# Performance work log

Hardware: AMD Instinct MI355X
Metric: run time of the kernel (lower is better)

Reference implementation:

```python
import jax, jax.numpy as jnp
import numpy as np

H = 16      # num_attention_heads
D = 64      # attention_head_size
HID = H * D # hidden_size = 1024
N = 1024    # seq_len == max_len
K = 1024    # position_buckets == att_span (K >= N so un-clamped indices stay in range)
EPS = 1e-7  # layer_norm_eps


def setup_inputs() -> dict:
    key = jax.random.key(0)
    ks = jax.random.split(key, 12)

    def w(k, shape):
        return jax.random.normal(k, shape, dtype=jnp.float32) * 0.02

    return {
        "hidden_states": jax.random.normal(ks[0], (1, N, HID), dtype=jnp.float32),
        "rel_embeddings": jax.random.normal(ks[1], (2 * K, HID), dtype=jnp.float32),
        "Wq": w(ks[2], (HID, HID)), "bq": jnp.zeros((HID,), jnp.float32),
        "Wk": w(ks[3], (HID, HID)), "bk": jnp.zeros((HID,), jnp.float32),
        "Wv": w(ks[4], (HID, HID)), "bv": jnp.zeros((HID,), jnp.float32),
        "Wpk": w(ks[5], (HID, HID)), "bpk": jnp.zeros((HID,), jnp.float32),
        "Wpq": w(ks[6], (HID, HID)), "bpq": jnp.zeros((HID,), jnp.float32),
        "Wo": w(ks[7], (HID, HID)), "bo": jnp.zeros((HID,), jnp.float32),
        "ln_g": jnp.ones((HID,), jnp.float32),
        "ln_b": jnp.zeros((HID,), jnp.float32),
    }


def _heads(x):
    # (L, HID) -> (H, L, D)   (batch size is 1, matching the baked-in id offsets)
    L = x.shape[0]
    return x.reshape(L, H, D).transpose(1, 0, 2)


def reference(hidden_states, rel_embeddings, Wq, bq, Wk, bk, Wv, bv,
              Wpk, bpk, Wpq, bpq, Wo, bo, ln_g, ln_b):
    hs = hidden_states[0]                       # (N, HID)
    q = _heads(hs @ Wq.T + bq)                  # (H, N, D)
    k = _heads(hs @ Wk.T + bk)                  # (H, N, D)
    v = _heads(hs @ Wv.T + bv)                  # (H, N, D)

    scale = jnp.sqrt(jnp.asarray(D * 3, jnp.float32))  # scale_factor = 1 + c2p + p2c = 3
    scores = jnp.einsum('hid,hjd->hij', q, k) / scale  # (H, N, N)

    pos_k = _heads(rel_embeddings @ Wpk.T + bpk)       # (H, 2K, D)
    pos_q = _heads(rel_embeddings @ Wpq.T + bpq)       # (H, 2K, D)

    rows = jnp.arange(N)[:, None]                      # (N, 1)
    # ids[i, j] = (i - j) + K  (no clamp in the original; valid since K >= N)
    idx = K + jnp.arange(N)[:, None] - jnp.arange(N)[None, :]  # (N, N)

    # c2p: gather c2p_att[h, i, K + i - j]
    c2p_att = jnp.einsum('hid,hkd->hik', q, pos_k)     # (H, N, 2K)
    c2p = c2p_att[:, rows, idx]                        # (H, N, N)

    # p2c: gather p2c_att[h, i, K + j - i], then transpose last two dims
    p2c_att = jnp.einsum('hid,hkd->hik', k, pos_q)     # (H, N, 2K)
    p2c = jnp.swapaxes(p2c_att[:, rows, idx.T], -1, -2)  # (H, N, N)

    scores = scores + (c2p + p2c) / scale
    attn = jax.nn.softmax(scores, axis=-1)             # (H, N, N)

    ctx = jnp.einsum('hij,hjd->hid', attn, v)          # (H, N, D)
    ctx = ctx.transpose(1, 0, 2).reshape(1, N, HID)    # (1, N, HID)

    # DebertaV2SelfOutput: dense + residual LayerNorm
    out = ctx @ Wo.T + bo
    x = out + hidden_states
    mu = jnp.mean(x, axis=-1, keepdims=True)
    var = jnp.mean(jnp.square(x - mu), axis=-1, keepdims=True)
    return ((x - mu) / jnp.sqrt(var + EPS)) * ln_g + ln_b
```

## Files before the change

kernel.cpp:

```cpp
#include <hip/hip_runtime.h>
#include <stdint.h>

#define HID 1024
#define NSEQ 1024
#define KREL 1024
#define NHEAD 16
#define DHEAD 64

typedef __attribute__((ext_vector_type(8))) short bhalf8;
typedef __attribute__((ext_vector_type(4))) float floatx4;

typedef const __attribute__((address_space(1))) uint8_t* gas_t;
typedef __attribute__((address_space(3))) uint8_t* las_t;
__device__ inline void gload16(const void* g, void* l) {
  __builtin_amdgcn_global_load_lds((gas_t)g, (las_t)l, 16, 0, 0);
}

__device__ inline uint16_t f2bf(float f) {
  union { float f; uint32_t u; } c; c.f = f;
  uint32_t u = c.u;
  return (uint16_t)((u + 0x7fffu + ((u >> 16) & 1u)) >> 16);
}
__device__ inline uint32_t pkbf(float a, float b) {
  union { float f; uint32_t u; } x, y; x.f = a; y.f = b;
#if __has_builtin(__builtin_amdgcn_perm)
  return __builtin_amdgcn_perm(x.u + 0x8000u, y.u + 0x8000u, 0x03020706u);
#else
  return ((x.u + 0x8000u) >> 16) | ((y.u + 0x8000u) & 0xffff0000u);
#endif
}

struct Cast8 {
  const float* src[8];
  uint16_t* dst[8];
  int n[8];
};
__global__ __launch_bounds__(256) void cast8_kernel(Cast8 c) {
  int seg = blockIdx.y;
  int n = c.n[seg];
  const float* s = c.src[seg];
  uint16_t* d = c.dst[seg];
  for (int idx = (blockIdx.x * 256 + threadIdx.x) * 4; idx < n; idx += 1024 * 256 * 4) {
    float4 v = *(const float4*)(s + idx);
    ushort4 o;
    o.x = f2bf(v.x); o.y = f2bf(v.y); o.z = f2bf(v.z); o.w = f2bf(v.w);
    *(ushort4*)(d + idx) = o;
  }
}

struct ProjArgs {
  const uint16_t* A[5];
  const uint16_t* W[5];
  const float* bias[5];
  uint16_t* C[5];
  int trans[5];
};
__global__ __launch_bounds__(256) void proj_gemm(ProjArgs pa) {
  __shared__ uint16_t a_s[2][128 * 32];
  __shared__ uint16_t b_s[2][128 * 32];
  int bidx = blockIdx.x;
  int xcd = bidx & 7, idx = bidx >> 3;
  int g = xcd * 7 + (idx >> 3);
  int nt = idx & 7;
  int z, mt;
  if (g < 24) { z = g >> 3; mt = g & 7; }
  else { int g2 = g - 24; z = 3 + (g2 >> 4); mt = g2 & 15; }
  const uint16_t* A = pa.A[z];
  const uint16_t* W = pa.W[z];
  int i0 = mt * 128, n0 = nt * 128;

  int t = threadIdx.x;
  int lane = t & 63, w = t >> 6;
  int fm = lane & 15, kq = lane >> 4;
  int wm = (w >> 1) * 64, wn = (w & 1) * 64;

  int lr = t >> 2, lc = (t & 3) * 8;
  const uint16_t* Agl = A + (size_t)(i0 + lr) * HID + lc;
  const uint16_t* Wgl = W + (size_t)(n0 + lr) * HID + lc;
  int lofs = t * 8;

#define PSTAGE(BUF, K0)                                                    \
  do {                                                                     \
    gload16(Agl + (K0), &a_s[BUF][lofs]);                                  \
    gload16(Agl + (K0) + 64 * HID, &a_s[BUF][lofs + 2048]);                \
    gload16(Wgl + (K0), &b_s[BUF][lofs]);                                  \
    gload16(Wgl + (K0) + 64 * HID, &b_s[BUF][lofs + 2048]);                \
  } while (0)

  floatx4 acc[4][4] = {};

  PSTAGE(0, 0);
  __syncthreads();

  for (int kt = 0; kt < 32; ++kt) {
    int cur = kt & 1;
    if (kt < 31) PSTAGE(cur ^ 1, (kt + 1) * 32);
    const uint16_t* as = &a_s[cur][0];
    const uint16_t* bs = &b_s[cur][0];
    bhalf8 af[4], bf[4];
#pragma unroll
    for (int m2 = 0; m2 < 4; ++m2)
      af[m2] = *(bhalf8*)(as + (wm + m2 * 16 + fm) * 32 + kq * 8);
#pragma unroll
    for (int n2 = 0; n2 < 4; ++n2)
      bf[n2] = *(bhalf8*)(bs + (wn + n2 * 16 + fm) * 32 + kq * 8);
#pragma unroll
    for (int m2 = 0; m2 < 4; ++m2)
#pragma unroll
      for (int n2 = 0; n2 < 4; ++n2)
        acc[m2][n2] = __builtin_amdgcn_mfma_f32_16x16x32_bf16(af[m2], bf[n2], acc[m2][n2], 0, 0, 0);
    __syncthreads();
  }
#undef PSTAGE

  const float* bias = pa.bias[z];
  uint16_t* C = pa.C[z];
  int tr = pa.trans[z];
#pragma unroll
  for (int m2 = 0; m2 < 4; ++m2) {
    int rowb = i0 + wm + m2 * 16 + kq * 4;
#pragma unroll
    for (int n2 = 0; n2 < 4; ++n2) {
      int col = n0 + wn + n2 * 16 + fm;
      float bv = bias[col];
      floatx4 v = acc[m2][n2];
      if (tr) {
        uint2 p = { pkbf(v[0] + bv, v[1] + bv), pkbf(v[2] + bv, v[3] + bv) };
        *(uint2*)(C + (size_t)col * NSEQ + rowb) = p;
      } else {
#pragma unroll
        for (int r = 0; r < 4; ++r)
          C[(size_t)(rowb + r) * HID + col] = f2bf(v[r] + bv);
      }
    }
  }
}

__global__ __launch_bounds__(256) void out_gemm(const uint16_t* __restrict__ Abf,
                                                const uint16_t* __restrict__ W,
                                                const float* __restrict__ bias,
                                                float* __restrict__ C) {
  __shared__ uint16_t a_s[2][64 * 32];
  __shared__ uint16_t b_s[2][64 * 32];
  int bidx = blockIdx.x;
  int i0 = (bidx >> 4) * 64, n0 = (bidx & 15) * 64;
  int t = threadIdx.x;
  int lane = t & 63, w = t >> 6;
  int fm = lane & 15, kq = lane >> 4;
  int wm = (w >> 1) * 32, wn = (w & 1) * 32;
  int lr = t >> 2, lc = (t & 3) * 8;
  const uint16_t* Agl = Abf + (size_t)(i0 + lr) * HID + lc;
  const uint16_t* Wgl = W + (size_t)(n0 + lr) * HID + lc;
  int lofs = t * 8;

#define OSTAGE(BUF, K0)                                                    \
  do {                                                                     \
    gload16(Agl + (K0), &a_s[BUF][lofs]);                                  \
    gload16(Wgl + (K0), &b_s[BUF][lofs]);                                  \
  } while (0)

  floatx4 acc00 = {0,0,0,0}, acc01 = {0,0,0,0}, acc10 = {0,0,0,0}, acc11 = {0,0,0,0};
  OSTAGE(0, 0);
  __syncthreads();
  for (int kt = 0; kt < 32; ++kt) {
    int cur = kt & 1;
    if (kt < 31) OSTAGE(cur ^ 1, (kt + 1) * 32);
    const uint16_t* as = &a_s[cur][0];
    const uint16_t* bs = &b_s[cur][0];
    bhalf8 a0 = *(bhalf8*)(as + (wm + fm) * 32 + kq * 8);
    bhalf8 a1 = *(bhalf8*)(as + (wm + 16 + fm) * 32 + kq * 8);
    bhalf8 b0 = *(bhalf8*)(bs + (wn + fm) * 32 + kq * 8);
    bhalf8 b1 = *(bhalf8*)(bs + (wn + 16 + fm) * 32 + kq * 8);
    acc00 = __builtin_amdgcn_mfma_f32_16x16x32_bf16(a0, b0, acc00, 0, 0, 0);
    acc01 = __builtin_amdgcn_mfma_f32_16x16x32_bf16(a0, b1, acc01, 0, 0, 0);
    acc10 = __builtin_amdgcn_mfma_f32_16x16x32_bf16(a1, b0, acc10, 0, 0, 0);
    acc11 = __builtin_amdgcn_mfma_f32_16x16x32_bf16(a1, b1, acc11, 0, 0, 0);
    __syncthreads();
  }
#undef OSTAGE
  int rb0 = kq * 4;
#define EPO(ACC, SM, SN)                                                   \
  {                                                                        \
    int rowb = i0 + wm + (SM)*16 + rb0;                                    \
    int col = n0 + wn + (SN)*16 + fm;                                      \
    float bv_ = bias[col];                                                 \
    _Pragma("unroll")                                                      \
    for (int rr = 0; rr < 4; ++rr)                                         \
      C[(size_t)(rowb + rr) * HID + col] = ACC[rr] + bv_;                  \
  }
  EPO(acc00, 0, 0) EPO(acc01, 0, 1) EPO(acc10, 1, 0) EPO(acc11, 1, 1)
#undef EPO
}

__global__ __launch_bounds__(256) void attn_kernel(const uint16_t* __restrict__ qg,
                                                   const uint16_t* __restrict__ kg,
                                                   const uint16_t* __restrict__ vtg,
                                                   const uint16_t* __restrict__ pkg,
                                                   const uint16_t* __restrict__ pqg,
                                                   uint16_t* __restrict__ ctx) {
  const float RSCALE = 0.07216878364870323f;
  __shared__ uint16_t Qs[32][72];
  __shared__ uint16_t Ks[32][72];
  __shared__ uint16_t Vt[64][40];
  __shared__ float C2Ps[2][32][68];
  __shared__ float P2C[2][32][68];
  __shared__ float Sqk[2][32][36];
  __shared__ uint16_t Pbf[32][40];
  __shared__ float m_sm[32], l_sm[32], al_sm[32];

  int t = threadIdx.x;
  int lane = t & 63, w = t >> 6;
  int fm = lane & 15;
  int kq = lane >> 4;

  int b = blockIdx.x;
  int xcd = b & 7, slot = b >> 3;
  int h = xcd * 2 + (slot & 1);
  int i0 = (slot >> 1) * 32;
  int cb = h * DHEAD;

  {
    int r = t >> 3, chq = (t & 7) * 8;
    *(uint4*)(&Qs[r][chq]) = *(const uint4*)(qg + (size_t)(i0 + r) * HID + cb + chq);
  }
  if (t < 32) { m_sm[t] = -1e30f; l_sm[t] = 0.f; }

  floatx4 opv0 = {0,0,0,0}, opv1 = {0,0,0,0};
  int wn = w * 16;
  int smt = w >> 1, snt = w & 1;
  int i2 = t >> 3, jj4 = (t & 7) * 4;

  int pr = t >> 3, pch = (t & 7) * 8;
  int rV = t >> 2, cV = (t & 3) * 8;
  const uint16_t* kb = kg + cb + pch;
  const uint16_t* vb = vtg + (size_t)(cb + rV) * HID + cV;

  int ntb = (w & 1) * 2;
  int brow_f = ntb * 16 + fm;
  const uint16_t* bgp = ((w < 2) ? pkg : pqg) + cb + kq * 8;
  int cbase = 31 - brow_f + kq * 4;

  uint4 rk, rv;
  bhalf8 nbA0, nbA1, nbB0, nbB1;

#define STAGE1(BUF, BA0, BA1, BB0, BB1)                                          \
  do {                                                                           \
    if (w < 2) {                                                                 \
      _Pragma("unroll")                                                          \
      for (int mt = 0; mt < 2; ++mt) {                                           \
        bhalf8 a0 = *(bhalf8*)(&Qs[mt * 16 + fm][kq * 8]);                       \
        bhalf8 a1 = *(bhalf8*)(&Qs[mt * 16 + fm][kq * 8 + 32]);                  \
        floatx4 ac0 = {0,0,0,0}, ac1 = {0,0,0,0};                                \
        ac0 = __builtin_amdgcn_mfma_f32_16x16x32_bf16(a0, BA0, ac0, 0, 0, 0);    \
        ac0 = __builtin_amdgcn_mfma_f32_16x16x32_bf16(a1, BA1, ac0, 0, 0, 0);    \
        ac1 = __builtin_amdgcn_mfma_f32_16x16x32_bf16(a0, BB0, ac1, 0, 0, 0);    \
        ac1 = __builtin_amdgcn_mfma_f32_16x16x32_bf16(a1, BB1, ac1, 0, 0, 0);    \
        _Pragma("unroll")                                                        \
        for (int r = 0; r < 4; ++r) {                                            \
          int i = mt * 16 + kq * 4 + r;                                          \
          C2Ps[BUF][i][(cbase + mt * 16 + r) & 63] = ac0[r];                     \
          C2Ps[BUF][i][(cbase + mt * 16 + r - 16) & 63] = ac1[r];                \
        }                                                                        \
      }                                                                          \
    } else {                                                                     \
      _Pragma("unroll")                                                          \
      for (int mt = 0; mt < 2; ++mt) {                                           \
        bhalf8 a0 = *(bhalf8*)(&Ks[mt * 16 + fm][kq * 8]);                       \
        bhalf8 a1 = *(bhalf8*)(&Ks[mt * 16 + fm][kq * 8 + 32]);                  \
        floatx4 ac0 = {0,0,0,0}, ac1 = {0,0,0,0};                                \
        ac0 = __builtin_amdgcn_mfma_f32_16x16x32_bf16(a0, BA0, ac0, 0, 0, 0);    \
        ac0 = __builtin_amdgcn_mfma_f32_16x16x32_bf16(a1, BA1, ac0, 0, 0, 0);    \
        ac1 = __builtin_amdgcn_mfma_f32_16x16x32_bf16(a0, BB0, ac1, 0, 0, 0);    \
        ac1 = __builtin_amdgcn_mfma_f32_16x16x32_bf16(a1, BB1, ac1, 0, 0, 0);    \
        _Pragma("unroll")                                                        \
        for (int r = 0; r < 4; ++r) {                                            \
          int jr = mt * 16 + kq * 4 + r;                                         \
          P2C[BUF][jr][brow_f] = ac0[r];                                         \
          P2C[BUF][jr][brow_f + 16] = ac1[r];                                    \
        }                                                                        \
      }                                                                          \
    }                                                                            \
    {                                                                            \
      bhalf8 qa0 = *(bhalf8*)(&Qs[smt * 16 + fm][kq * 8]);                       \
      bhalf8 qa1 = *(bhalf8*)(&Qs[smt * 16 + fm][kq * 8 + 32]);                  \
      bhalf8 kb0 = *(bhalf8*)(&Ks[snt * 16 + fm][kq * 8]);                       \
      bhalf8 kb1 = *(bhalf8*)(&Ks[snt * 16 + fm][kq * 8 + 32]);                  \
      floatx4 sacc = {0,0,0,0};                                                  \
      sacc = __builtin_amdgcn_mfma_f32_16x16x32_bf16(qa0, kb0, sacc, 0, 0, 0);   \
      sacc = __builtin_amdgcn_mfma_f32_16x16x32_bf16(qa1, kb1, sacc, 0, 0, 0);   \
      _Pragma("unroll")                                                          \
      for (int r = 0; r < 4; ++r)                                                \
        Sqk[BUF][smt * 16 + kq * 4 + r][snt * 16 + fm] = sacc[r];                \
    }                                                                            \
  } while (0)

  rk = *(const uint4*)(kb);
  rv = *(const uint4*)(vb);
  *(uint4*)(&Ks[pr][pch]) = rk;
  *(uint4*)(&Vt[rV][cV]) = rv;
  __syncthreads();
  rk = *(const uint4*)(kb + (size_t)(32 + pr) * HID);
  rv = *(const uint4*)(vb + 32);
  {
    int rbase = KREL + i0 - 31;
    int r0 = rbase + brow_f;      if (r0 > 2047) r0 = 2047;
    int r1 = rbase + brow_f + 16; if (r1 > 2047) r1 = 2047;
    bhalf8 tA0 = *(const bhalf8*)(bgp + ((size_t)r0 << 10));
    bhalf8 tA1 = *(const bhalf8*)(bgp + ((size_t)r0 << 10) + 32);
    bhalf8 tB0 = *(const bhalf8*)(bgp + ((size_t)r1 << 10));
    bhalf8 tB1 = *(const bhalf8*)(bgp + ((size_t)r1 << 10) + 32);
    STAGE1(0, tA0, tA1, tB0, tB1);
  }
  __syncthreads();
  {
    *(uint4*)(&Ks[pr][pch]) = rk;
    rk = *(const uint4*)(kb + (size_t)(64 + pr) * HID);
    int rb1 = KREL + i0 - 63;
    int r0 = rb1 + brow_f;
    nbA0 = *(const bhalf8*)(bgp + ((size_t)r0 << 10));
    nbA1 = *(const bhalf8*)(bgp + ((size_t)r0 << 10) + 32);
    nbB0 = *(const bhalf8*)(bgp + ((size_t)(r0 + 16) << 10));
    nbB1 = *(const bhalf8*)(bgp + ((size_t)(r0 + 16) << 10) + 32);
  }
  __syncthreads();

  for (int jt = 0; jt < NSEQ / 32; ++jt) {
    int cur = jt & 1;

    float4 v_sqk = *(const float4*)(&Sqk[cur][i2][jj4]);
    float4 v_c2p = *(const float4*)(&C2Ps[cur][i2][jj4]);
    float p0 = P2C[cur][jj4 + 0][i2 - jj4 + 31];
    float p1 = P2C[cur][jj4 + 1][i2 - jj4 + 30];
    float p2 = P2C[cur][jj4 + 2][i2 - jj4 + 29];
    float p3 = P2C[cur][jj4 + 3][i2 - jj4 + 28];

    if (jt < 31) {
      int bi = cur ^ 1;
      STAGE1(bi, nbA0, nbA1, nbB0, nbB1);
    }

    {
      float sv0 = (v_sqk.x + v_c2p.x + p0) * RSCALE;
      float sv1 = (v_sqk.y + v_c2p.y + p1) * RSCALE;
      float sv2 = (v_sqk.z + v_c2p.z + p2) * RSCALE;
      float sv3 = (v_sqk.w + v_c2p.w + p3) * RSCALE;
      float mx = fmaxf(fmaxf(sv0, sv1), fmaxf(sv2, sv3));
      mx = fmaxf(mx, __shfl_xor(mx, 1));
      mx = fmaxf(mx, __shfl_xor(mx, 2));
      mx = fmaxf(mx, __shfl_xor(mx, 4));
      float m_old = m_sm[i2];
      float m_new = fmaxf(m_old, mx);
      float al = __expf(m_old - m_new);
      float e0 = __expf(sv0 - m_new);
      float e1 = __expf(sv1 - m_new);
      float e2 = __expf(sv2 - m_new);
      float e3 = __expf(sv3 - m_new);
      uint2 pk2v;
      pk2v.x = (uint32_t)f2bf(e0) | ((uint32_t)f2bf(e1) << 16);
      pk2v.y = (uint32_t)f2bf(e2) | ((uint32_t)f2bf(e3) << 16);
      *(uint2*)(&Pbf[i2][jj4]) = pk2v;
      float ts = (e0 + e1) + (e2 + e3);
      ts += __shfl_xor(ts, 1);
      ts += __shfl_xor(ts, 2);
      ts += __shfl_xor(ts, 4);
      if (jj4 == 0) { m_sm[i2] = m_new; l_sm[i2] = l_sm[i2] * al + ts; al_sm[i2] = al; }
    }
    __syncthreads();

    {
      floatx4 al0 = *(const floatx4*)(&al_sm[kq * 4]);
      floatx4 al1 = *(const floatx4*)(&al_sm[16 + kq * 4]);
#pragma unroll
      for (int r = 0; r < 4; ++r) {
        opv0[r] *= al0[r];
        opv1[r] *= al1[r];
      }
      bhalf8 vbf = *(bhalf8*)(&Vt[wn + fm][kq * 8]);
      bhalf8 pa0 = *(bhalf8*)(&Pbf[fm][kq * 8]);
      bhalf8 pa1 = *(bhalf8*)(&Pbf[16 + fm][kq * 8]);
      opv0 = __builtin_amdgcn_mfma_f32_16x16x32_bf16(pa0, vbf, opv0, 0, 0, 0);
      opv1 = __builtin_amdgcn_mfma_f32_16x16x32_bf16(pa1, vbf, opv1, 0, 0, 0);
      if (jt < 31) *(uint4*)(&Vt[rV][cV]) = rv;
      if (jt < 30) rv = *(const uint4*)(vb + (jt + 2) * 32);
    }
    if (jt < 30) {
      *(uint4*)(&Ks[pr][pch]) = rk;
    }
    if (jt < 29) {
      rk = *(const uint4*)(kb + (size_t)((jt + 3) * 32 + pr) * HID);
    }
    if (jt < 30) {
      int rb = KREL + i0 - (jt + 2) * 32 - 31;
      int r0 = rb + brow_f;
      nbA0 = *(const bhalf8*)(bgp + ((size_t)r0 << 10));
      nbA1 = *(const bhalf8*)(bgp + ((size_t)r0 << 10) + 32);
      nbB0 = *(const bhalf8*)(bgp + ((size_t)(r0 + 16) << 10));
      nbB1 = *(const bhalf8*)(bgp + ((size_t)(r0 + 16) << 10) + 32);
    }
    __syncthreads();
  }
#undef STAGE1

  {
    floatx4 l0 = *(const floatx4*)(&l_sm[kq * 4]);
    floatx4 l1 = *(const floatx4*)(&l_sm[16 + kq * 4]);
#pragma unroll
    for (int r = 0; r < 4; ++r) {
      int ia = kq * 4 + r, ib = 16 + kq * 4 + r;
      ctx[(size_t)(i0 + ia) * HID + cb + wn + fm] = f2bf(opv0[r] / l0[r]);
      ctx[(size_t)(i0 + ib) * HID + cb + wn + fm] = f2bf(opv1[r] / l1[r]);
    }
  }
}

__global__ __launch_bounds__(256) void ln_kernel(const float* __restrict__ xin,
                                                 const float* __restrict__ hs,
                                                 const float* __restrict__ g,
                                                 const float* __restrict__ b,
                                                 float* __restrict__ y) {
  int row = blockIdx.x, t = threadIdx.x;
  int c = t * 4;
  float4 a = *(const float4*)(xin + (size_t)row * HID + c);
  float4 hv = *(const float4*)(hs + (size_t)row * HID + c);
  float x0 = a.x + hv.x, x1 = a.y + hv.y, x2 = a.z + hv.z, x3 = a.w + hv.w;
  float s = x0 + x1 + x2 + x3;
  float sq = x0 * x0 + x1 * x1 + x2 * x2 + x3 * x3;
  for (int off = 32; off; off >>= 1) {
    s += __shfl_xor(s, off);
    sq += __shfl_xor(sq, off);
  }
  __shared__ float rs[4], rq[4];
  int w = t >> 6, lane = t & 63;
  if (lane == 0) { rs[w] = s; rq[w] = sq; }
  __syncthreads();
  s = rs[0] + rs[1] + rs[2] + rs[3];
  sq = rq[0] + rq[1] + rq[2] + rq[3];
  float mu = s * (1.0f / HID);
  float var = sq * (1.0f / HID) - mu * mu;
  float rstd = rsqrtf(var + 1e-7f);
  float4 gg = *(const float4*)(g + c);
  float4 bb = *(const float4*)(b + c);
  float4 out;
  out.x = (x0 - mu) * rstd * gg.x + bb.x;
  out.y = (x1 - mu) * rstd * gg.y + bb.y;
  out.z = (x2 - mu) * rstd * gg.z + bb.z;
  out.w = (x3 - mu) * rstd * gg.w + bb.w;
  *(float4*)(y + (size_t)row * HID + c) = out;
}

extern "C" void kernel_launch(void* const* d_in, const int* in_sizes, int n_in,
                              void* d_out, int out_size, void* d_ws, size_t ws_size,
                              hipStream_t stream) {
  const float* hs  = (const float*)d_in[0];
  const float* rel = (const float*)d_in[1];
  const float* Wq  = (const float*)d_in[2];  const float* bq  = (const float*)d_in[3];
  const float* Wk  = (const float*)d_in[4];  const float* bk  = (const float*)d_in[5];
  const float* Wv  = (const float*)d_in[6];  const float* bv  = (const float*)d_in[7];
  const float* Wpk = (const float*)d_in[8];  const float* bpk = (const float*)d_in[9];
  const float* Wpq = (const float*)d_in[10]; const float* bpq = (const float*)d_in[11];
  const float* Wo  = (const float*)d_in[12]; const float* bo  = (const float*)d_in[13];
  const float* lng = (const float*)d_in[14]; const float* lnb = (const float*)d_in[15];

  char* ws = (char*)d_ws;
  const size_t MB = 1024 * 1024;
  uint16_t* q_bf   = (uint16_t*)(ws + 0 * MB);
  uint16_t* k_bf   = (uint16_t*)(ws + 2 * MB);
  uint16_t* vt_bf  = (uint16_t*)(ws + 4 * MB);
  uint16_t* pk_bf  = (uint16_t*)(ws + 6 * MB);
  uint16_t* pq_bf  = (uint16_t*)(ws + 10 * MB);
  uint16_t* ctx_bf = (uint16_t*)(ws + 14 * MB);
  float*    out_f  = (float*)   (ws + 16 * MB);
  uint16_t* hs_bf  = (uint16_t*)(ws + 20 * MB);
  uint16_t* rel_bf = (uint16_t*)(ws + 22 * MB);
  uint16_t* Wq_bf  = (uint16_t*)(ws + 26 * MB);
  uint16_t* Wk_bf  = (uint16_t*)(ws + 28 * MB);
  uint16_t* Wv_bf  = (uint16_t*)(ws + 30 * MB);
  uint16_t* Wpk_bf = (uint16_t*)(ws + 32 * MB);
  uint16_t* Wpq_bf = (uint16_t*)(ws + 34 * MB);
  uint16_t* Wo_bf  = (uint16_t*)(ws + 36 * MB);

  dim3 blk(256);

  Cast8 c8;
  c8.src[0] = hs;  c8.dst[0] = hs_bf;  c8.n[0] = 1024 * 1024;
  c8.src[1] = rel; c8.dst[1] = rel_bf; c8.n[1] = 2048 * 1024;
  c8.src[2] = Wq;  c8.dst[2] = Wq_bf;  c8.n[2] = 1024 * 1024;
  c8.src[3] = Wk;  c8.dst[3] = Wk_bf;  c8.n[3] = 1024 * 1024;
  c8.src[4] = Wv;  c8.dst[4] = Wv_bf;  c8.n[4] = 1024 * 1024;
  c8.src[5] = Wpk; c8.dst[5] = Wpk_bf; c8.n[5] = 1024 * 1024;
  c8.src[6] = Wpq; c8.dst[6] = Wpq_bf; c8.n[6] = 1024 * 1024;
  c8.src[7] = Wo;  c8.dst[7] = Wo_bf;  c8.n[7] = 1024 * 1024;
  cast8_kernel<<<dim3(1024, 8), blk, 0, stream>>>(c8);

  ProjArgs pa;
  pa.A[0] = hs_bf;  pa.A[1] = hs_bf;  pa.A[2] = hs_bf;  pa.A[3] = rel_bf; pa.A[4] = rel_bf;
  pa.W[0] = Wq_bf;  pa.W[1] = Wk_bf;  pa.W[2] = Wv_bf;  pa.W[3] = Wpk_bf; pa.W[4] = Wpq_bf;
  pa.bias[0] = bq;  pa.bias[1] = bk;  pa.bias[2] = bv;  pa.bias[3] = bpk; pa.bias[4] = bpq;
  pa.C[0] = q_bf; pa.C[1] = k_bf; pa.C[2] = vt_bf; pa.C[3] = pk_bf; pa.C[4] = pq_bf;
  pa.trans[0] = 0; pa.trans[1] = 0; pa.trans[2] = 1; pa.trans[3] = 0; pa.trans[4] = 0;
  proj_gemm<<<dim3(448), blk, 0, stream>>>(pa);

  attn_kernel<<<dim3(512), blk, 0, stream>>>(q_bf, k_bf, vt_bf, pk_bf, pq_bf, ctx_bf);

  out_gemm<<<dim3(256), blk, 0, stream>>>(ctx_bf, Wo_bf, bo, out_f);

  ln_kernel<<<dim3(1024), blk, 0, stream>>>(out_f, hs, lng, lnb, (float*)d_out);
}
```

Before: 204.8 us.

## Load GEMM operands directly from global memory instead of LDS staging

The projection and output GEMMs no longer stage A and W tiles through double-buffered shared memory with global_load_lds. Each lane now reads its bf16x8 MFMA fragments straight from global memory, which removes the LDS traffic and the per-iteration barriers. In exchange, operand reuse across waves now depends on the L1/L2 caches, and the scattered 16-byte row reads lose coalescing and software prefetch, so the loads may become latency-bound.

```diff
diff --git a/kernel.cpp b/kernel.cpp
--- a/kernel.cpp
+++ b/kernel.cpp
@@ -9,12 +9,6 @@
 
 typedef __attribute__((ext_vector_type(8))) short bhalf8;
 typedef __attribute__((ext_vector_type(4))) float floatx4;
-
-typedef const __attribute__((address_space(1))) uint8_t* gas_t;
-typedef __attribute__((address_space(3))) uint8_t* las_t;
-__device__ inline void gload16(const void* g, void* l) {
-  __builtin_amdgcn_global_load_lds((gas_t)g, (las_t)l, 16, 0, 0);
-}
 
 __device__ inline uint16_t f2bf(float f) {
   union { float f; uint32_t u; } c; c.f = f;
@@ -56,8 +50,6 @@
   int trans[5];
 };
 __global__ __launch_bounds__(256) void proj_gemm(ProjArgs pa) {
-  __shared__ uint16_t a_s[2][128 * 32];
-  __shared__ uint16_t b_s[2][128 * 32];
   int bidx = blockIdx.x;
   int xcd = bidx & 7, idx = bidx >> 3;
   int g = xcd * 7 + (idx >> 3);
@@ -74,44 +66,26 @@
   int fm = lane & 15, kq = lane >> 4;
   int wm = (w >> 1) * 64, wn = (w & 1) * 64;
 
-  int lr = t >> 2, lc = (t & 3) * 8;
-  const uint16_t* Agl = A + (size_t)(i0 + lr) * HID + lc;
-  const uint16_t* Wgl = W + (size_t)(n0 + lr) * HID + lc;
-  int lofs = t * 8;
-
-#define PSTAGE(BUF, K0)                                                    \
-  do {                                                                     \
-    gload16(Agl + (K0), &a_s[BUF][lofs]);                                  \
-    gload16(Agl + (K0) + 64 * HID, &a_s[BUF][lofs + 2048]);                \
-    gload16(Wgl + (K0), &b_s[BUF][lofs]);                                  \
-    gload16(Wgl + (K0) + 64 * HID, &b_s[BUF][lofs + 2048]);                \
-  } while (0)
+  const uint16_t* Ab = A + (size_t)(i0 + wm + fm) * HID + kq * 8;
+  const uint16_t* Wb = W + (size_t)(n0 + wn + fm) * HID + kq * 8;
 
   floatx4 acc[4][4] = {};
 
-  PSTAGE(0, 0);
-  __syncthreads();
-
   for (int kt = 0; kt < 32; ++kt) {
-    int cur = kt & 1;
-    if (kt < 31) PSTAGE(cur ^ 1, (kt + 1) * 32);
-    const uint16_t* as = &a_s[cur][0];
-    const uint16_t* bs = &b_s[cur][0];
+    int ko = kt * 32;
     bhalf8 af[4], bf[4];
 #pragma unroll
     for (int m2 = 0; m2 < 4; ++m2)
-      af[m2] = *(bhalf8*)(as + (wm + m2 * 16 + fm) * 32 + kq * 8);
+      af[m2] = *(const bhalf8*)(Ab + (size_t)(m2 * 16) * HID + ko);
 #pragma unroll
     for (int n2 = 0; n2 < 4; ++n2)
-      bf[n2] = *(bhalf8*)(bs + (wn + n2 * 16 + fm) * 32 + kq * 8);
+      bf[n2] = *(const bhalf8*)(Wb + (size_t)(n2 * 16) * HID + ko);
 #pragma unroll
     for (int m2 = 0; m2 < 4; ++m2)
 #pragma unroll
       for (int n2 = 0; n2 < 4; ++n2)
         acc[m2][n2] = __builtin_amdgcn_mfma_f32_16x16x32_bf16(af[m2], bf[n2], acc[m2][n2], 0, 0, 0);
-    __syncthreads();
-  }
-#undef PSTAGE
+  }
 
   const float* bias = pa.bias[z];
   uint16_t* C = pa.C[z];
@@ -140,44 +114,26 @@
                                                 const uint16_t* __restrict__ W,
                                                 const float* __restrict__ bias,
                                                 float* __restrict__ C) {
-  __shared__ uint16_t a_s[2][64 * 32];
-  __shared__ uint16_t b_s[2][64 * 32];
   int bidx = blockIdx.x;
   int i0 = (bidx >> 4) * 64, n0 = (bidx & 15) * 64;
   int t = threadIdx.x;
   int lane = t & 63, w = t >> 6;
   int fm = lane & 15, kq = lane >> 4;
   int wm = (w >> 1) * 32, wn = (w & 1) * 32;
-  int lr = t >> 2, lc = (t & 3) * 8;
-  const uint16_t* Agl = Abf + (size_t)(i0 + lr) * HID + lc;
-  const uint16_t* Wgl = W + (size_t)(n0 + lr) * HID + lc;
-  int lofs = t * 8;
-
-#define OSTAGE(BUF, K0)                                                    \
-  do {                                                                     \
-    gload16(Agl + (K0), &a_s[BUF][lofs]);                                  \
-    gload16(Wgl + (K0), &b_s[BUF][lofs]);                                  \
-  } while (0)
-
+  const uint16_t* Ab = Abf + (size_t)(i0 + wm + fm) * HID + kq * 8;
+  const uint16_t* Wb = W + (size_t)(n0 + wn + fm) * HID + kq * 8;
   floatx4 acc00 = {0,0,0,0}, acc01 = {0,0,0,0}, acc10 = {0,0,0,0}, acc11 = {0,0,0,0};
-  OSTAGE(0, 0);
-  __syncthreads();
   for (int kt = 0; kt < 32; ++kt) {
-    int cur = kt & 1;
-    if (kt < 31) OSTAGE(cur ^ 1, (kt + 1) * 32);
-    const uint16_t* as = &a_s[cur][0];
-    const uint16_t* bs = &b_s[cur][0];
-    bhalf8 a0 = *(bhalf8*)(as + (wm + fm) * 32 + kq * 8);
-    bhalf8 a1 = *(bhalf8*)(as + (wm + 16 + fm) * 32 + kq * 8);
-    bhalf8 b0 = *(bhalf8*)(bs + (wn + fm) * 32 + kq * 8);
-    bhalf8 b1 = *(bhalf8*)(bs + (wn + 16 + fm) * 32 + kq * 8);
+    int ko = kt * 32;
+    bhalf8 a0 = *(const bhalf8*)(Ab + ko);
+    bhalf8 a1 = *(const bhalf8*)(Ab + (size_t)16 * HID + ko);
+    bhalf8 b0 = *(const bhalf8*)(Wb + ko);
+    bhalf8 b1 = *(const bhalf8*)(Wb + (size_t)16 * HID + ko);
     acc00 = __builtin_amdgcn_mfma_f32_16x16x32_bf16(a0, b0, acc00, 0, 0, 0);
     acc01 = __builtin_amdgcn_mfma_f32_16x16x32_bf16(a0, b1, acc01, 0, 0, 0);
     acc10 = __builtin_amdgcn_mfma_f32_16x16x32_bf16(a1, b0, acc10, 0, 0, 0);
     acc11 = __builtin_amdgcn_mfma_f32_16x16x32_bf16(a1, b1, acc11, 0, 0, 0);
-    __syncthreads();
-  }
-#undef OSTAGE
+  }
   int rb0 = kq * 4;
 #define EPO(ACC, SM, SN)                                                   \
   {                                                                        \
```

After: 239.8 us. +17.0%, slower.
